# Performance work log

Hardware: AMD Instinct MI355X
Metric: run time of the kernel (lower is better)

The kernel has to match this reference:

```python
import jax, jax.numpy as jnp
import numpy as np

EPS = 0.1        # entropic regularization
MAX_ITER = 50    # max Sinkhorn iterations
THRESH = 0.1     # early-stop threshold on |u - u1|


def setup_inputs() -> dict:
    key = jax.random.key(0)
    kx, ky = jax.random.split(key)
    x = jax.random.normal(kx, (4, 3072, 32), dtype=jnp.float32)
    y = jax.random.normal(ky, (4, 3072, 32), dtype=jnp.float32)
    return {"x": x, "y": y}


def _sinkhorn(x, y):
    B, P1, _ = x.shape
    P2 = y.shape[1]
    x2 = jnp.sum(x * x, axis=-1)                       # [B, P1]
    y2 = jnp.sum(y * y, axis=-1)                       # [B, P2]
    C = x2[:, :, None] + y2[:, None, :] - 2.0 * jnp.einsum('bid,bjd->bij', x, y)  # [B,P1,P2]

    log_mu = jnp.log(jnp.float32(1.0 / P1) + 1e-8)     # uniform marginals
    log_nu = jnp.log(jnp.float32(1.0 / P2) + 1e-8)

    def M(u, v):
        # modified cost M_ij = (-C_ij + u_i + v_j) / eps
        return (-C + u[:, :, None] + v[:, None, :]) / EPS

    def step(carry, _):
        u, v, done = carry
        u_new = EPS * (log_mu - jax.nn.logsumexp(M(u, v), axis=-1)) + u
        v_new = EPS * (log_nu - jax.nn.logsumexp(M(u_new, v), axis=-2)) + v
        err = jnp.mean(jnp.sum(jnp.abs(u_new - u), axis=-1))
        # freeze updates once converged (emulates the torch early break)
        u_out = jnp.where(done, u, u_new)
        v_out = jnp.where(done, v, v_new)
        done = done | (err < THRESH)
        return (u_out, v_out, done), None

    u0 = jnp.zeros((B, P1), dtype=C.dtype)
    v0 = jnp.zeros((B, P2), dtype=C.dtype)
    (u, v, _), _ = jax.lax.scan(jax.checkpoint(step), (u0, v0, jnp.array(False)),
                                None, length=MAX_ITER)

    pi = jnp.exp(M(u, v))                              # transport plan [B,P1,P2]
    cost = jnp.sum(pi * C, axis=(-2, -1))              # [B]  (reduction='none')
    return cost, pi, C


def reference(x, y):
    return _sinkhorn(x, y)
```

## Files before the change

kernel.cpp:

```cpp
#include <hip/hip_runtime.h>
#include <math.h>

#define BATCH 4
#define P 3072
#define NROW (BATCH * P)
#define NTILE (NROW / 16)
#define TPB (P / 16)
#define MAXIT 50
#define NBLK 256
#define RPB 48
#define CTW 24

#define LN2 0.69314718055994531f
#define INV_LN2 1.44269504088896341f

typedef _Float16 f16x8 __attribute__((ext_vector_type(8)));
typedef float f32x4 __attribute__((ext_vector_type(4)));

__device__ inline float waveReduceSum(float v) {
#pragma unroll
  for (int off = 32; off > 0; off >>= 1) v += __shfl_xor(v, off, 64);
  return v;
}
__device__ inline float fexp2(float x) { return __builtin_amdgcn_exp2f(x); }
__device__ inline float flog2(float x) { return __builtin_amdgcn_logf(x); }

__device__ inline float cohLoad(const float* p) {
  return __hip_atomic_load(p, __ATOMIC_RELAXED, __HIP_MEMORY_SCOPE_AGENT);
}
__device__ inline void cohStore(float* p, float val) {
  __hip_atomic_store(p, val, __ATOMIC_RELAXED, __HIP_MEMORY_SCOPE_AGENT);
}
__device__ inline int cohLoadI(const int* p) {
  return __hip_atomic_load(p, __ATOMIC_RELAXED, __HIP_MEMORY_SCOPE_AGENT);
}
__device__ inline void cohStoreI(int* p, int val) {
  __hip_atomic_store(p, val, __ATOMIC_RELAXED, __HIP_MEMORY_SCOPE_AGENT);
}

__device__ inline void gridBarrier(int* bar, int target) {
  __syncthreads();
  if (threadIdx.x == 0) {
    __builtin_amdgcn_sched_barrier(0);
    int g = blockIdx.x >> 4;
    int old = __hip_atomic_fetch_add(&bar[g * 16], 1, __ATOMIC_RELAXED,
                                     __HIP_MEMORY_SCOPE_AGENT);
    if ((old & 15) == 15) {
      int r = __hip_atomic_fetch_add(&bar[256], 1, __ATOMIC_RELAXED,
                                     __HIP_MEMORY_SCOPE_AGENT);
      if ((r & 15) == 15)
        cohStoreI(&bar[272], target);
    }
    while (cohLoadI(&bar[272]) < target) __builtin_amdgcn_s_sleep(1);
    __builtin_amdgcn_sched_barrier(0);
  }
  __syncthreads();
}

__global__ __launch_bounds__(256) void prep_kernel(const float* __restrict__ x,
                                                   const float* __restrict__ y,
                                                   _Float16* __restrict__ xh,
                                                   _Float16* __restrict__ yh,
                                                   float* __restrict__ x2,
                                                   float* __restrict__ y2,
                                                   float* __restrict__ vb) {
  int t = threadIdx.x;
  int lane = t & 63;
  int g = lane >> 4, r = lane & 15;
  int tileG = blockIdx.x * 4 + (t >> 6);
  int isY = tileG >= NTILE;
  int tile = isY ? (tileG - NTILE) : tileG;
  const float* src = isY ? y : x;
  int row = tile * 16 + r;
  const float* p = src + (size_t)row * 32 + g * 8;
  float4 v0 = *(const float4*)p;
  float4 v1 = *(const float4*)(p + 4);
  float sq = v0.x * v0.x + v0.y * v0.y + v0.z * v0.z + v0.w * v0.w +
             v1.x * v1.x + v1.y * v1.y + v1.z * v1.z + v1.w * v1.w;
  sq += __shfl_xor(sq, 16, 64);
  sq += __shfl_xor(sq, 32, 64);
  float scale = isY ? 1.0f : 20.0f * INV_LN2;
  f16x8 h;
  h[0] = (_Float16)(scale * v0.x); h[1] = (_Float16)(scale * v0.y);
  h[2] = (_Float16)(scale * v0.z); h[3] = (_Float16)(scale * v0.w);
  h[4] = (_Float16)(scale * v1.x); h[5] = (_Float16)(scale * v1.y);
  h[6] = (_Float16)(scale * v1.z); h[7] = (_Float16)(scale * v1.w);
  _Float16* dst = (isY ? yh : xh) + (size_t)tile * 512 + lane * 8;
  *(f16x8*)dst = h;
  if (lane < 16) {
    if (isY) { y2[row] = sq; vb[row] = -10.0f * INV_LN2 * sq; }
    else     { x2[row] = sq; }
  }
}

__global__ __launch_bounds__(512, 2) void sinkhorn_kernel(
    const _Float16* __restrict__ xh, const _Float16* __restrict__ yh,
    float* __restrict__ u, float* __restrict__ v,
    float* __restrict__ ub, float* __restrict__ vb,
    const float* __restrict__ x2, const float* __restrict__ y2,
    float* __restrict__ errpart, int* __restrict__ bar, float lmn) {
  int tid = threadIdx.x;
  int lane = tid & 63;
  int w = tid >> 6;
  int rsel = lane & 15;
  int g = lane >> 4;
  int bid = blockIdx.x;
  int b = bid >> 6;
  int tile0 = bid * 3;
  int gr0 = bid * RPB;
  f16x8 xfr[3], yfr[3];
#pragma unroll
  for (int rt = 0; rt < 3; ++rt) {
    xfr[rt] = *(const f16x8*)(xh + (size_t)(tile0 + rt) * 512 + lane * 8);
    yfr[rt] = *(const f16x8*)(yh + (size_t)(tile0 + rt) * 512 + lane * 8);
  }
  size_t jbase = ((size_t)(b * TPB + w * CTW)) * 512 + lane * 8;
  const _Float16* BxP = xh + jbase;
  const _Float16* ByP = yh + jbase;
  int sboff = w * (CTW * 16) + rsel;

  __shared__ float sb[P];
  __shared__ float lm[8][RPB], ls[8][RPB];
  __shared__ int sdone;

  auto stageBias = [&](const float* biasIn) {
    const float* bp = biasIn + b * P;
#pragma unroll
    for (int k = 0; k < 6; ++k) sb[tid + k * 512] = cohLoad(&bp[tid + k * 512]);
    __syncthreads();
  };

  auto halfstep_online = [&](const f16x8* afr, const _Float16* Bp,
                             const float* nrm, float* pot, float* biasOut, bool trackErr) {
    float m[3][4], s[3][4];
#pragma unroll
    for (int rt = 0; rt < 3; ++rt)
#pragma unroll
      for (int r = 0; r < 4; ++r) { m[rt][r] = -1e30f; s[rt][r] = 0.f; }
#pragma unroll 2
    for (int c = 0; c < 6; ++c) {
      f16x8 bfr[4];
      float bb[4];
#pragma unroll
      for (int t4 = 0; t4 < 4; ++t4) {
        bfr[t4] = *(const f16x8*)(Bp + ((size_t)(c * 4 + t4) << 9));
        bb[t4] = sb[sboff + (c * 4 + t4) * 16];
      }
#pragma unroll
      for (int rt = 0; rt < 3; ++rt) {
        f32x4 acc[4];
#pragma unroll
        for (int t4 = 0; t4 < 4; ++t4) {
          f32x4 ci = {bb[t4], bb[t4], bb[t4], bb[t4]};
          acc[t4] = __builtin_amdgcn_mfma_f32_16x16x32_f16(afr[rt], bfr[t4], ci, 0, 0, 0);
        }
#pragma unroll
        for (int r = 0; r < 4; ++r) {
          float a0 = acc[0][r], a1 = acc[1][r], a2 = acc[2][r], a3 = acc[3][r];
          float cm = fmaxf(fmaxf(a0, a1), fmaxf(a2, a3));
          float nm = fmaxf(m[rt][r], cm);
          s[rt][r] = s[rt][r] * fexp2(m[rt][r] - nm) +
                     fexp2(a0 - nm) + fexp2(a1 - nm) + fexp2(a2 - nm) + fexp2(a3 - nm);
          m[rt][r] = nm;
        }
      }
    }
#pragma unroll
    for (int rt = 0; rt < 3; ++rt)
#pragma unroll
      for (int r = 0; r < 4; ++r) {
#pragma unroll
        for (int o = 1; o < 16; o <<= 1) {
          float om = __shfl_xor(m[rt][r], o, 64);
          float os = __shfl_xor(s[rt][r], o, 64);
          float nm = fmaxf(m[rt][r], om);
          s[rt][r] = s[rt][r] * fexp2(m[rt][r] - nm) + os * fexp2(om - nm);
          m[rt][r] = nm;
        }
      }
    __syncthreads();
    if (rsel == 0) {
#pragma unroll
      for (int rt = 0; rt < 3; ++rt)
#pragma unroll
        for (int r = 0; r < 4; ++r) {
          lm[w][rt * 16 + g * 4 + r] = m[rt][r];
          ls[w][rt * 16 + g * 4 + r] = s[rt][r];
        }
    }
    __syncthreads();
    float e = 0.f;
    if (tid < RPB) {
      float M = lm[0][tid], S = ls[0][tid];
#pragma unroll
      for (int w2 = 1; w2 < 8; ++w2) {
        float om = lm[w2][tid], os = ls[w2][tid];
        float nm = fmaxf(M, om);
        S = S * fexp2(M - nm) + os * fexp2(om - nm);
        M = nm;
      }
      float L2v = M + flog2(S);
      int gi = gr0 + tid;
      float nv = 0.1f * lmn + nrm[gi] - 0.1f * LN2 * L2v;
      if (trackErr) e = fabsf(nv - pot[gi]);
      pot[gi] = nv;
      cohStore(&biasOut[gi], 10.0f * INV_LN2 * (nv - nrm[gi]));
    }
    if (trackErr && tid < 64) {
      e = waveReduceSum(e);
      if (tid == 0) cohStore(&errpart[bid], e);
    }
  };

  auto halfstep_fast = [&](const f16x8* afr, const _Float16* Bp,
                           const float* nrm, float* pot, float* biasOut, bool trackErr) {
    float off[3][4];
#pragma unroll
    for (int rt = 0; rt < 3; ++rt)
#pragma unroll
      for (int r = 0; r < 4; ++r) {
        int row = gr0 + rt * 16 + g * 4 + r;
        off[rt][r] = 10.0f * INV_LN2 * (0.1f * lmn + nrm[row] - pot[row]);
      }
    float s[3][4];
#pragma unroll
    for (int rt = 0; rt < 3; ++rt)
#pragma unroll
      for (int r = 0; r < 4; ++r) s[rt][r] = 0.f;
#pragma unroll 2
    for (int c = 0; c < 6; ++c) {
      f16x8 bfr[4];
      float bb[4];
#pragma unroll
      for (int t4 = 0; t4 < 4; ++t4) {
        bfr[t4] = *(const f16x8*)(Bp + ((size_t)(c * 4 + t4) << 9));
        bb[t4] = sb[sboff + (c * 4 + t4) * 16];
      }
#pragma unroll
      for (int rt = 0; rt < 3; ++rt) {
        f32x4 acc[4];
#pragma unroll
        for (int t4 = 0; t4 < 4; ++t4) {
          f32x4 ci = {bb[t4] - off[rt][0], bb[t4] - off[rt][1],
                      bb[t4] - off[rt][2], bb[t4] - off[rt][3]};
          acc[t4] = __builtin_amdgcn_mfma_f32_16x16x32_f16(afr[rt], bfr[t4], ci, 0, 0, 0);
        }
#pragma unroll
        for (int r = 0; r < 4; ++r)
          s[rt][r] += (fexp2(acc[0][r]) + fexp2(acc[1][r])) +
                      (fexp2(acc[2][r]) + fexp2(acc[3][r]));
      }
    }
#pragma unroll
    for (int rt = 0; rt < 3; ++rt)
#pragma unroll
      for (int r = 0; r < 4; ++r) {
#pragma unroll
        for (int o = 1; o < 16; o <<= 1)
          s[rt][r] += __shfl_xor(s[rt][r], o, 64);
      }
    __syncthreads();
    if (rsel == 0) {
#pragma unroll
      for (int rt = 0; rt < 3; ++rt)
#pragma unroll
        for (int r = 0; r < 4; ++r) ls[w][rt * 16 + g * 4 + r] = s[rt][r];
    }
    __syncthreads();
    float e = 0.f;
    if (tid < RPB) {
      float S = ls[0][tid];
#pragma unroll
      for (int w2 = 1; w2 < 8; ++w2) S += ls[w2][tid];
      int gi = gr0 + tid;
      float po = pot[gi];
      float nv = po - 0.1f * LN2 * flog2(S);
      if (trackErr) e = fabsf(nv - po);
      pot[gi] = nv;
      cohStore(&biasOut[gi], 10.0f * INV_LN2 * (nv - nrm[gi]));
    }
    if (trackErr && tid < 64) {
      e = waveReduceSum(e);
      if (tid == 0) cohStore(&errpart[bid], e);
    }
  };

  int ep = 0;
  for (int it = 0; it < MAXIT; ++it) {
    stageBias(vb);
    if (it == 0) halfstep_online(xfr, ByP, x2, u, ub, true);
    else         halfstep_fast(xfr, ByP, x2, u, ub, true);
    gridBarrier(bar, ++ep);
    if (bid == 0 && tid < 64) {
      float ts = cohLoad(&errpart[tid]) + cohLoad(&errpart[tid + 64]) +
                 cohLoad(&errpart[tid + 128]) + cohLoad(&errpart[tid + 192]);
      ts = waveReduceSum(ts);
      if (tid == 0) cohStoreI(&bar[288], (ts * 0.25f < 0.1f) ? 1 : 0);
    }
    stageBias(ub);
    if (it == 0) halfstep_online(yfr, BxP, y2, v, vb, false);
    else         halfstep_fast(yfr, BxP, y2, v, vb, false);
    gridBarrier(bar, ++ep);
    if (tid == 0) sdone = cohLoadI(&bar[288]);
    __syncthreads();
    if (sdone) break;
  }
}

__global__ __launch_bounds__(256) void final_kernel(const float* __restrict__ x,
                                                    const float* __restrict__ y,
                                                    const float* __restrict__ x2,
                                                    const float* __restrict__ y2,
                                                    const float* __restrict__ u,
                                                    const float* __restrict__ v,
                                                    float* __restrict__ C,
                                                    float* __restrict__ pi,
                                                    float* __restrict__ costpart) {
  __shared__ float xs[64][33];
  __shared__ float ys[64][33];
  int t = threadIdx.x;
  int b = blockIdx.z;
  int i0 = blockIdx.x * 64;
  int j0 = blockIdx.y * 64;
  const float4* xg = (const float4*)(x + ((size_t)b * P + i0) * 32);
  const float4* yg = (const float4*)(y + ((size_t)b * P + j0) * 32);
#pragma unroll
  for (int k = 0; k < 2; ++k) {
    int f4 = t + k * 256;
    int row = f4 >> 3;
    int col = (f4 & 7) << 2;
    float4 xv = xg[f4];
    xs[row][col] = xv.x; xs[row][col + 1] = xv.y; xs[row][col + 2] = xv.z; xs[row][col + 3] = xv.w;
    float4 yv = yg[f4];
    ys[row][col] = yv.x; ys[row][col + 1] = yv.y; ys[row][col + 2] = yv.z; ys[row][col + 3] = yv.w;
  }
  __syncthreads();
  int ti = t >> 4, tj = t & 15;
  int ib = ti * 4, jb = tj * 4;
  float acc[4][4];
#pragma unroll
  for (int a = 0; a < 4; ++a)
#pragma unroll
    for (int bb = 0; bb < 4; ++bb) acc[a][bb] = 0.f;
#pragma unroll 8
  for (int k = 0; k < 32; ++k) {
    float xa[4], yb[4];
#pragma unroll
    for (int a = 0; a < 4; ++a) xa[a] = xs[ib + a][k];
#pragma unroll
    for (int bb = 0; bb < 4; ++bb) yb[bb] = ys[jb + bb][k];
#pragma unroll
    for (int a = 0; a < 4; ++a)
#pragma unroll
      for (int bb = 0; bb < 4; ++bb) acc[a][bb] = fmaf(xa[a], yb[bb], acc[a][bb]);
  }
  float y2r[4], vr[4];
#pragma unroll
  for (int bb = 0; bb < 4; ++bb) {
    y2r[bb] = y2[b * P + j0 + jb + bb];
    vr[bb] = v[b * P + j0 + jb + bb];
  }
  float costacc = 0.f;
#pragma unroll
  for (int a = 0; a < 4; ++a) {
    int gi = b * P + i0 + ib + a;
    float x2r = x2[gi];
    float ur = u[gi];
    float4 co, po;
    co.x = x2r + y2r[0] - 2.f * acc[a][0];
    co.y = x2r + y2r[1] - 2.f * acc[a][1];
    co.z = x2r + y2r[2] - 2.f * acc[a][2];
    co.w = x2r + y2r[3] - 2.f * acc[a][3];
    po.x = __expf((ur + vr[0] - co.x) * 10.f);
    po.y = __expf((ur + vr[1] - co.y) * 10.f);
    po.z = __expf((ur + vr[2] - co.z) * 10.f);
    po.w = __expf((ur + vr[3] - co.w) * 10.f);
    costacc += po.x * co.x + po.y * co.y + po.z * co.z + po.w * co.w;
    float* crow = C + (size_t)gi * P + j0;
    ((float4*)crow)[tj] = co;
    float* prow = pi + (size_t)gi * P + j0;
    ((float4*)prow)[tj] = po;
  }
  costacc = waveReduceSum(costacc);
  __shared__ float red[4];
  if ((t & 63) == 0) red[t >> 6] = costacc;
  __syncthreads();
  if (t == 0)
    costpart[((size_t)b * 48 + blockIdx.y) * 48 + blockIdx.x] =
        red[0] + red[1] + red[2] + red[3];
}

__global__ __launch_bounds__(256) void cost_kernel(const float* __restrict__ costpart,
                                                   float* __restrict__ cost) {
  __shared__ float red[4];
  int t = threadIdx.x;
  for (int b = 0; b < BATCH; ++b) {
    float loc = 0.f;
    for (int idx = t; idx < 2304; idx += 256) loc += costpart[b * 2304 + idx];
    loc = waveReduceSum(loc);
    if ((t & 63) == 0) red[t >> 6] = loc;
    __syncthreads();
    if (t == 0) cost[b] = red[0] + red[1] + red[2] + red[3];
    __syncthreads();
  }
}

extern "C" void kernel_launch(void* const* d_in, const int* in_sizes, int n_in,
                              void* d_out, int out_size, void* d_ws, size_t ws_size,
                              hipStream_t stream) {
  (void)in_sizes; (void)n_in; (void)out_size; (void)ws_size;
  const float* x = (const float*)d_in[0];
  const float* y = (const float*)d_in[1];
  float* out = (float*)d_out;
  float* cost = out;
  float* pi = out + 4;
  float* C = pi + (size_t)BATCH * P * P;

  float* u = (float*)d_ws;
  int* bar = (int*)(u + NROW);
  float* v = (float*)(bar + 512);
  float* ub = v + NROW;
  float* vb = ub + NROW;
  float* x2 = vb + NROW;
  float* y2 = x2 + NROW;
  float* errpart = y2 + NROW;
  float* costpart = errpart + NBLK;

  _Float16* xh = (_Float16*)C;
  _Float16* yh = xh + (size_t)NROW * 32;

  hipMemsetAsync(d_ws, 0, (size_t)NROW * sizeof(float) + 512 * sizeof(int), stream);

  float lmn = logf(1.0f / 3072.0f + 1e-8f);

  prep_kernel<<<384, 256, 0, stream>>>(x, y, xh, yh, x2, y2, vb);
  sinkhorn_kernel<<<NBLK, 512, 0, stream>>>(xh, yh, u, v, ub, vb, x2, y2,
                                            errpart, bar, lmn);
  final_kernel<<<dim3(48, 48, 4), 256, 0, stream>>>(x, y, x2, y2, u, v, C, pi, costpart);
  cost_kernel<<<1, 256, 0, stream>>>(costpart, cost);
}
```

Measured before the change: 1.570 ms.

## Replace grid-wide barrier with per-batch barriers and async convergence flag

```diff
diff --git a/kernel.cpp b/kernel.cpp
--- a/kernel.cpp
+++ b/kernel.cpp
@@ -9,6 +9,7 @@
 #define MAXIT 50
 #define NBLK 256
 #define RPB 48
+#define WAVES 8
 #define CTW 24
 
 #define LN2 0.69314718055994531f
@@ -38,20 +39,20 @@
   __hip_atomic_store(p, val, __ATOMIC_RELAXED, __HIP_MEMORY_SCOPE_AGENT);
 }
 
-__device__ inline void gridBarrier(int* bar, int target) {
+__device__ inline void batchBarrier(int* bb, int target, int local) {
   __syncthreads();
   if (threadIdx.x == 0) {
     __builtin_amdgcn_sched_barrier(0);
-    int g = blockIdx.x >> 4;
-    int old = __hip_atomic_fetch_add(&bar[g * 16], 1, __ATOMIC_RELAXED,
+    int g = local >> 3;
+    int old = __hip_atomic_fetch_add(&bb[g * 16], 1, __ATOMIC_RELAXED,
                                      __HIP_MEMORY_SCOPE_AGENT);
-    if ((old & 15) == 15) {
-      int r = __hip_atomic_fetch_add(&bar[256], 1, __ATOMIC_RELAXED,
+    if ((old & 7) == 7) {
+      int r = __hip_atomic_fetch_add(&bb[128], 1, __ATOMIC_RELAXED,
                                      __HIP_MEMORY_SCOPE_AGENT);
-      if ((r & 15) == 15)
-        cohStoreI(&bar[272], target);
-    }
-    while (cohLoadI(&bar[272]) < target) __builtin_amdgcn_s_sleep(1);
+      if ((r & 7) == 7)
+        cohStoreI(&bb[144], target);
+    }
+    while (cohLoadI(&bb[144]) < target) __builtin_amdgcn_s_sleep(1);
     __builtin_amdgcn_sched_barrier(0);
   }
   __syncthreads();
@@ -98,7 +99,9 @@
     float* __restrict__ u, float* __restrict__ v,
     float* __restrict__ ub, float* __restrict__ vb,
     const float* __restrict__ x2, const float* __restrict__ y2,
-    float* __restrict__ errpart, int* __restrict__ bar, float lmn) {
+    float* __restrict__ errpart, int* __restrict__ bar,
+    int* __restrict__ gcount, int* __restrict__ gdone,
+    float* __restrict__ berr, float lmn) {
   int tid = threadIdx.x;
   int lane = tid & 63;
   int w = tid >> 6;
@@ -106,6 +109,8 @@
   int g = lane >> 4;
   int bid = blockIdx.x;
   int b = bid >> 6;
+  int local = bid & 63;
+  int* bbar = bar + b * 256;
   int tile0 = bid * 3;
   int gr0 = bid * RPB;
   f16x8 xfr[3], yfr[3];
@@ -120,7 +125,7 @@
   int sboff = w * (CTW * 16) + rsel;
 
   __shared__ float sb[P];
-  __shared__ float lm[8][RPB], ls[8][RPB];
+  __shared__ float lm[WAVES][RPB], ls[WAVES][RPB];
   __shared__ int sdone;
 
   auto stageBias = [&](const float* biasIn) {
@@ -193,7 +198,7 @@
     if (tid < RPB) {
       float M = lm[0][tid], S = ls[0][tid];
 #pragma unroll
-      for (int w2 = 1; w2 < 8; ++w2) {
+      for (int w2 = 1; w2 < WAVES; ++w2) {
         float om = lm[w2][tid], os = ls[w2][tid];
         float nm = fmaxf(M, om);
         S = S * fexp2(M - nm) + os * fexp2(om - nm);
@@ -271,7 +276,7 @@
     if (tid < RPB) {
       float S = ls[0][tid];
 #pragma unroll
-      for (int w2 = 1; w2 < 8; ++w2) S += ls[w2][tid];
+      for (int w2 = 1; w2 < WAVES; ++w2) S += ls[w2][tid];
       int gi = gr0 + tid;
       float po = pot[gi];
       float nv = po - 0.1f * LN2 * flog2(S);
@@ -290,18 +295,31 @@
     stageBias(vb);
     if (it == 0) halfstep_online(xfr, ByP, x2, u, ub, true);
     else         halfstep_fast(xfr, ByP, x2, u, ub, true);
-    gridBarrier(bar, ++ep);
-    if (bid == 0 && tid < 64) {
-      float ts = cohLoad(&errpart[tid]) + cohLoad(&errpart[tid + 64]) +
-                 cohLoad(&errpart[tid + 128]) + cohLoad(&errpart[tid + 192]);
-      ts = waveReduceSum(ts);
-      if (tid == 0) cohStoreI(&bar[288], (ts * 0.25f < 0.1f) ? 1 : 0);
+    batchBarrier(bbar, ++ep, local);
+    if (local == 0 && tid < 64) {
+      float e = cohLoad(&errpart[b * 64 + tid]);
+      e = waveReduceSum(e);
+      if (tid == 0) {
+        cohStore(&berr[b], e);
+        asm volatile("s_waitcnt vmcnt(0)");
+        int r = __hip_atomic_fetch_add(&gcount[it], 1, __ATOMIC_RELAXED,
+                                       __HIP_MEMORY_SCOPE_AGENT);
+        if (r == 3) {
+          float ts = cohLoad(&berr[0]) + cohLoad(&berr[1]) +
+                     cohLoad(&berr[2]) + cohLoad(&berr[3]);
+          cohStoreI(&gdone[it], (ts * 0.25f < 0.1f) ? 2 : 1);
+        }
+      }
     }
     stageBias(ub);
     if (it == 0) halfstep_online(yfr, BxP, y2, v, vb, false);
     else         halfstep_fast(yfr, BxP, y2, v, vb, false);
-    gridBarrier(bar, ++ep);
-    if (tid == 0) sdone = cohLoadI(&bar[288]);
+    batchBarrier(bbar, ++ep, local);
+    if (tid == 0) {
+      int gd;
+      while ((gd = cohLoadI(&gdone[it])) == 0) __builtin_amdgcn_s_sleep(1);
+      sdone = (gd == 2);
+    }
     __syncthreads();
     if (sdone) break;
   }
@@ -418,7 +436,10 @@
 
   float* u = (float*)d_ws;
   int* bar = (int*)(u + NROW);
-  float* v = (float*)(bar + 512);
+  int* gcount = bar + 1024;
+  int* gdone = gcount + 64;
+  float* berr = (float*)(gdone + 64);
+  float* v = berr + 4;
   float* ub = v + NROW;
   float* vb = ub + NROW;
   float* x2 = vb + NROW;
@@ -429,13 +450,13 @@
   _Float16* xh = (_Float16*)C;
   _Float16* yh = xh + (size_t)NROW * 32;
 
-  hipMemsetAsync(d_ws, 0, (size_t)NROW * sizeof(float) + 512 * sizeof(int), stream);
+  hipMemsetAsync(d_ws, 0, (size_t)NROW * sizeof(float) + 4624, stream);
 
   float lmn = logf(1.0f / 3072.0f + 1e-8f);
 
   prep_kernel<<<384, 256, 0, stream>>>(x, y, xh, yh, x2, y2, vb);
   sinkhorn_kernel<<<NBLK, 512, 0, stream>>>(xh, yh, u, v, ub, vb, x2, y2,
-                                            errpart, bar, lmn);
+                                            errpart, bar, gcount, gdone, berr, lmn);
   final_kernel<<<dim3(48, 48, 4), 256, 0, stream>>>(x, y, x2, y2, u, v, C, pi, costpart);
   cost_kernel<<<1, 256, 0, stream>>>(costpart, cost);
 }
```

Measured after the change: 1.429 ms. 1.1x faster.
